# Kernel optimization log

Hardware: AMD Instinct MI355X
Metric: run time of the kernel (lower is better)

The kernel has to match this reference:

```python
import jax, jax.numpy as jnp
import numpy as np

B, S, HID = 2, 2048, 3584
NH, NKV, HD = 16, 8, 256
WINDOW = 1024
SOFTCAP = 50.0


def setup_inputs() -> dict:
    key = jax.random.key(0)
    ks = jax.random.split(key, 8)
    hidden_states = jax.random.normal(ks[0], (B, S, HID), dtype=jnp.float32)
    attention_mask = jnp.ones((B, S), dtype=bool)
    position_ids = jnp.tile(jnp.arange(S, dtype=jnp.int32), (B, 1))
    # rotary tables indexed by position, last dim = head_dim
    inv_freq = 1.0 / (10000.0 ** (jnp.arange(0, HD, 2, dtype=jnp.float32) / HD))
    t = jnp.arange(S, dtype=jnp.float32)
    freqs = jnp.outer(t, inv_freq)  # [S, HD/2]
    emb = jnp.concatenate([freqs, freqs], axis=-1)  # [S, HD]
    sin, cos = jnp.sin(emb), jnp.cos(emb)
    causal_mask = jnp.tril(jnp.ones((1, 1, S, S), dtype=bool))
    sc = 0.02
    Wq = jax.random.normal(ks[1], (HID, NH * HD), dtype=jnp.float32) * sc
    Wk = jax.random.normal(ks[2], (HID, NKV * HD), dtype=jnp.float32) * sc
    Wv = jax.random.normal(ks[3], (HID, NKV * HD), dtype=jnp.float32) * sc
    Wo = jax.random.normal(ks[4], (NH * HD, HID), dtype=jnp.float32) * sc
    return {"hidden_states": hidden_states, "attention_mask": attention_mask,
            "position_ids": position_ids, "sin": sin, "cos": cos,
            "causal_mask": causal_mask, "Wq": Wq, "Wk": Wk, "Wv": Wv, "Wo": Wo}


def _rotate_half(x):
    x1, x2 = x[..., : x.shape[-1] // 2], x[..., x.shape[-1] // 2 :]
    return jnp.concatenate((-x2, x1), axis=-1)


def reference(hidden_states, attention_mask, position_ids, sin, cos, causal_mask, Wq, Wk, Wv, Wo):
    b, s, _ = hidden_states.shape
    q = (hidden_states @ Wq).reshape(b, s, NH, HD)
    k = (hidden_states @ Wk).reshape(b, s, NKV, HD)
    v = (hidden_states @ Wv).reshape(b, s, NKV, HD)

    # RoPE, applied in [b, h, s, d] layout as in the original
    s_ = sin[position_ids][:, None, :, :]  # [b,1,s,d]
    c_ = cos[position_ids][:, None, :, :]
    qh = q.transpose(0, 2, 1, 3)
    kh = k.transpose(0, 2, 1, 3)
    qh = qh * c_ + _rotate_half(qh) * s_
    kh = kh * c_ + _rotate_half(kh) * s_
    q = qh.transpose(0, 2, 1, 3)  # [b,s,nh,d]
    k = kh.transpose(0, 2, 1, 3)  # [b,s,nkv,d]

    # GQA: repeat kv heads to match query heads
    groups = NH // NKV
    k = jnp.repeat(k, groups, axis=2)  # [b,s,nh,d]
    v = jnp.repeat(v, groups, axis=2)

    # combine causal + padding masks, then sliding-window (even layer)
    mask = causal_mask[:, :, :s, :s] & attention_mask[:, None, None, :]  # [b,1,s,s]
    mask = jnp.broadcast_to(mask, (b, 1, s, s))
    far_past = jnp.tril(jnp.ones((s, s), dtype=bool), k=-WINDOW)[None, None]
    mask = mask & ~far_past

    neg = jnp.finfo(jnp.float32).min
    bias = jnp.where(mask, 0.0, neg).astype(jnp.float32)

    scale = HD ** -0.5
    logits = jnp.einsum("bqhd,bkhd->bhqk", q, k) * scale
    # Gemma2 logit softcapping
    logits = SOFTCAP * jnp.tanh(logits / SOFTCAP)
    logits = logits + bias
    probs = jax.nn.softmax(logits, axis=-1)
    out = jnp.einsum("bhqk,bkhd->bqhd", probs, v)
    out = out.reshape(b, s, NH * HD)
    return out @ Wo
```

## Files before the change

kernel.cpp:

```cpp
#include <hip/hip_runtime.h>
#include <hip/hip_bf16.h>

typedef __bf16 bf16x8_t __attribute__((ext_vector_type(8)));
typedef __bf16 bf16x4_t __attribute__((ext_vector_type(4)));
typedef short s16x4_t  __attribute__((ext_vector_type(4)));
typedef float f32x4_t  __attribute__((ext_vector_type(4)));

#define NB 2
#define NS 2048
#define NHID 3584
#define NHEADS 16
#define NKVH 8
#define DH 256
#define WIN 1024

__device__ __forceinline__ float bf2f(ushort u) {
  union { unsigned v; float f; } x; x.v = ((unsigned)u) << 16; return x.f;
}
__device__ __forceinline__ ushort f2bf(float f) {
  unsigned x = __builtin_bit_cast(unsigned, f);
  unsigned r = (x + 0x7fffu + ((x >> 16) & 1u)) >> 16;
  return (ushort)r;
}

__device__ __forceinline__ void gload16(const void* g, void* l) {
  __builtin_amdgcn_global_load_lds((const __attribute__((address_space(1))) void*)g,
                                   (__attribute__((address_space(3))) void*)l, 16, 0, 0);
}

__device__ __forceinline__ f32x4_t mfma_pv(s16x4_t a, s16x4_t b, f32x4_t c) {
#if __has_builtin(__builtin_amdgcn_mfma_f32_16x16x16_bf16)
  return __builtin_amdgcn_mfma_f32_16x16x16_bf16(
      __builtin_bit_cast(bf16x4_t, a), __builtin_bit_cast(bf16x4_t, b), c, 0, 0, 0);
#else
  return __builtin_amdgcn_mfma_f32_16x16x16bf16_1k(a, b, c, 0, 0, 0);
#endif
}

__device__ __forceinline__ float pexp(float s) {
  float e = __expf(fminf(s * 0.0025f, 80.f));
  float th = __fdividef(e - 1.f, e + 1.f);
  return __expf(50.f * th);
}

__global__ __launch_bounds__(256) void f32_to_bf16_kernel(const float* __restrict__ in,
                                                          ushort* __restrict__ out, int n4) {
  int i = (int)blockIdx.x * 256 + (int)threadIdx.x;
  if (i < n4) {
    float4 v = ((const float4*)in)[i];
    ushort4 o;
    o.x = f2bf(v.x); o.y = f2bf(v.y); o.z = f2bf(v.z); o.w = f2bf(v.w);
    ((ushort4*)out)[i] = o;
  }
}

__global__ __launch_bounds__(256) void transpose_f32_bf16(const float* __restrict__ in,
                                                          ushort* __restrict__ out,
                                                          int R, int Cc) {
  __shared__ ushort tile[64][72];
  const int t = threadIdx.x;
  const int ct = Cc >> 6;
  const int by = blockIdx.x / ct;
  const int bx = blockIdx.x % ct;
  const int r0 = by << 6, c0 = bx << 6;
#pragma unroll
  for (int i = 0; i < 16; ++i) {
    int idx = i * 256 + t;
    int r = idx >> 6, c = idx & 63;
    tile[r][c] = f2bf(in[(size_t)(r0 + r) * Cc + c0 + c]);
  }
  __syncthreads();
#pragma unroll
  for (int i = 0; i < 16; ++i) {
    int idx = i * 256 + t;
    int rr = idx >> 6, cc = idx & 63;
    out[(size_t)(c0 + rr) * R + r0 + cc] = tile[cc][rr];
  }
}

#define GSYNC1 do { __builtin_amdgcn_s_barrier(); \
    asm volatile("s_waitcnt lgkmcnt(0)" ::: "memory"); \
    __builtin_amdgcn_sched_barrier(0); } while (0)
#define GSYNC2(st) do { \
    if (st) asm volatile("s_waitcnt vmcnt(2)" ::: "memory"); \
    else    asm volatile("s_waitcnt vmcnt(0)" ::: "memory"); \
    __builtin_amdgcn_sched_barrier(0); \
    __builtin_amdgcn_s_barrier(); } while (0)

template <int EPI>
__global__ __launch_bounds__(512, 2) void gemm256(const ushort* __restrict__ A,
                                                  const ushort* __restrict__ Bt,
                                                  void* __restrict__ Cout,
                                                  int M, int N, int K) {
  __shared__ alignas(16) char lds[131072];
  const int t = threadIdx.x;
  const int lane = t & 63;
  const int wid = t >> 6;
  const int wm = wid >> 2;
  const int wn = wid & 3;
  const int g = lane >> 4;
  const int lr = lane & 15;
  const int lrow8 = lane >> 3;
  const int lp = (lane & 7) ^ lrow8;

  const int nbn = N >> 8;
  const int nwg = (int)gridDim.x;
  const int bid = (int)blockIdx.x;
  const int swz = (bid & 7) * (nwg >> 3) + (bid >> 3);
  const int bm = swz / nbn, bn = swz % nbn;
  const int m0 = bm << 8, n0 = bn << 8;

  f32x4_t acc[8][4] = {};
  const int T = K >> 6;

  auto stageA = [&](int q, int koff, int bufn) {
    int row = (q << 6) + (wid << 3) + lrow8;
    gload16(A + (size_t)(m0 + row) * K + koff + (lp << 3),
            lds + bufn * 32768 + (q << 13) + (wid << 10));
  };
  auto stageB = [&](int q, int koff, int bufn) {
    int row = (q << 6) + (wid << 3) + lrow8;
    gload16(Bt + (size_t)(n0 + row) * K + koff + (lp << 3),
            lds + 65536 + bufn * 32768 + (q << 13) + (wid << 10));
  };

#pragma unroll
  for (int q = 0; q < 4; ++q) { stageA(q, 0, 0); stageB(q, 0, 0); }
  asm volatile("s_waitcnt vmcnt(0)" ::: "memory");
  __builtin_amdgcn_s_barrier();

  for (int tt = 0; tt < T; ++tt) {
    const int bc = tt & 1;
    const int bnx = bc ^ 1;
    const bool st = (tt + 1 < T);
    const int kn = (tt + 1) << 6;
    const char* cA = lds + bc * 32768;
    const char* cB = lds + 65536 + bc * 32768;
    bf16x8_t af[4], bfv[4];

    auto ldA = [&](int i, int mh, int ks) {
      int row = (wm << 7) + (mh << 6) + (i << 4) + lr;
      af[i] = *(const bf16x8_t*)(cA + (row << 7) + (((ks << 6) + (g << 4)) ^ ((row & 7) << 4)));
    };
    auto ldB = [&](int j, int ks) {
      int row = (wn << 6) + (j << 4) + lr;
      bfv[j] = *(const bf16x8_t*)(cB + (row << 7) + (((ks << 6) + (g << 4)) ^ ((row & 7) << 4)));
    };

#pragma unroll
    for (int i = 0; i < 4; ++i) ldA(i, 0, 0);
#pragma unroll
    for (int j = 0; j < 4; ++j) ldB(j, 0);
    if (st) { stageA(0, kn, bnx); stageA(2, kn, bnx); }
    GSYNC1;
    __builtin_amdgcn_s_setprio(1);
#pragma unroll
    for (int i = 0; i < 4; ++i)
#pragma unroll
      for (int j = 0; j < 4; ++j)
        acc[i][j] = __builtin_amdgcn_mfma_f32_16x16x32_bf16(af[i], bfv[j], acc[i][j], 0, 0, 0);
    __builtin_amdgcn_s_setprio(0);
    GSYNC2(st);

#pragma unroll
    for (int i = 0; i < 4; ++i) ldA(i, 1, 0);
    if (st) { stageB(0, kn, bnx); stageB(1, kn, bnx); }
    GSYNC1;
    __builtin_amdgcn_s_setprio(1);
#pragma unroll
    for (int i = 0; i < 4; ++i)
#pragma unroll
      for (int j = 0; j < 4; ++j)
        acc[4 + i][j] = __builtin_amdgcn_mfma_f32_16x16x32_bf16(af[i], bfv[j], acc[4 + i][j], 0, 0, 0);
    __builtin_amdgcn_s_setprio(0);
    GSYNC2(st);

#pragma unroll
    for (int i = 0; i < 4; ++i) ldA(i, 0, 1);
#pragma unroll
    for (int j = 0; j < 4; ++j) ldB(j, 1);
    if (st) { stageB(2, kn, bnx); stageB(3, kn, bnx); }
    GSYNC1;
    __builtin_amdgcn_s_setprio(1);
#pragma unroll
    for (int i = 0; i < 4; ++i)
#pragma unroll
      for (int j = 0; j < 4; ++j)
        acc[i][j] = __builtin_amdgcn_mfma_f32_16x16x32_bf16(af[i], bfv[j], acc[i][j], 0, 0, 0);
    __builtin_amdgcn_s_setprio(0);
    GSYNC2(st);

#pragma unroll
    for (int i = 0; i < 4; ++i) ldA(i, 1, 1);
    if (st) { stageA(1, kn, bnx); stageA(3, kn, bnx); }
    GSYNC1;
    __builtin_amdgcn_s_setprio(1);
#pragma unroll
    for (int i = 0; i < 4; ++i)
#pragma unroll
      for (int j = 0; j < 4; ++j)
        acc[4 + i][j] = __builtin_amdgcn_mfma_f32_16x16x32_bf16(af[i], bfv[j], acc[4 + i][j], 0, 0, 0);
    __builtin_amdgcn_s_setprio(0);
    GSYNC2(st);
  }

  __syncthreads();
  const bool trstage = (EPI == 4) && (n0 >= 2048);
  if (trstage) {
#pragma unroll
    for (int i = 0; i < 8; ++i)
#pragma unroll
      for (int j = 0; j < 4; ++j) {
        int col = (wn << 6) + (j << 4) + lr;
#pragma unroll
        for (int r = 0; r < 4; ++r) {
          int row = (wm << 7) + (i << 4) + (g << 2) + r;
          *(ushort*)(lds + (col << 9) + ((row << 1) ^ ((col & 7) << 4))) = f2bf(acc[i][j][r]);
        }
      }
  } else {
#pragma unroll
    for (int i = 0; i < 8; ++i)
#pragma unroll
      for (int j = 0; j < 4; ++j) {
        int col = (wn << 6) + (j << 4) + lr;
#pragma unroll
        for (int r = 0; r < 4; ++r) {
          int row = (wm << 7) + (i << 4) + (g << 2) + r;
          *(ushort*)(lds + (row << 9) + ((col << 1) ^ ((row & 7) << 4))) = f2bf(acc[i][j][r]);
        }
      }
  }
  __syncthreads();

  if (EPI == 0) {
    ushort* C = (ushort*)Cout;
#pragma unroll
    for (int it = 0; it < 16; ++it) {
      int idx = it * 512 + t;
      int row = idx >> 5, ch = idx & 31;
      uint4 v = *(const uint4*)(lds + (row << 9) + ((ch << 4) ^ ((row & 7) << 4)));
      *(uint4*)(C + (size_t)(m0 + row) * N + n0 + (ch << 3)) = v;
    }
  } else if (EPI == 4) {
    ushort* C = (ushort*)Cout;
    if (n0 < 2048) {
#pragma unroll
      for (int it = 0; it < 16; ++it) {
        int idx = it * 512 + t;
        int row = idx >> 5, ch = idx & 31;
        uint4 v = *(const uint4*)(lds + (row << 9) + ((ch << 4) ^ ((row & 7) << 4)));
        *(uint4*)(C + (size_t)(m0 + row) * 2048 + n0 + (ch << 3)) = v;
      }
    } else {
      ushort* vC = C + (size_t)4096 * 2048;
      const int plane = (m0 >> 11) * NKVH + ((n0 - 2048) >> 8);
      ushort* dst = vC + (size_t)plane * ((size_t)NS * DH) + (size_t)((m0 & (NS - 1)) >> 5) * 8192;
#pragma unroll
      for (int it = 0; it < 16; ++it) {
        int s = it * 512 + t;
        int lr2 = s & 7, kq = (s >> 3) & 7, dt_l = (s >> 6) & 15, sb_l = s >> 10;
        int d0 = (dt_l << 4) + (lr2 << 1);
        int r0 = (sb_l << 5) + (kq << 2);
        uint2 a = *(const uint2*)(lds + (d0 << 9) + ((r0 << 1) ^ ((d0 & 7) << 4)));
        uint2 b2 = *(const uint2*)(lds + ((d0 + 1) << 9) + ((r0 << 1) ^ (((d0 + 1) & 7) << 4)));
        uint4 v; v.x = a.x; v.y = a.y; v.z = b2.x; v.w = b2.y;
        *(uint4*)(dst + (size_t)s * 8) = v;
      }
    }
  } else {
    float* Cf = (float*)Cout;
#pragma unroll
    for (int it = 0; it < 32; ++it) {
      int idx = it * 512 + t;
      int row = idx >> 6, qd = idx & 63;
      ushort4 hv = *(const ushort4*)(lds + (row << 9) + ((qd << 3) ^ ((row & 7) << 4)));
      float4 fv;
      fv.x = bf2f(hv.x); fv.y = bf2f(hv.y); fv.z = bf2f(hv.z); fv.w = bf2f(hv.w);
      *(float4*)(Cf + (size_t)(m0 + row) * N + n0 + (qd << 2)) = fv;
    }
  }
}

__global__ __launch_bounds__(256) void rope_kernel(ushort* __restrict__ buf,
                                                   const float* __restrict__ sint,
                                                   const float* __restrict__ cost,
                                                   int nheads) {
  int idx = (int)blockIdx.x * 256 + (int)threadIdx.x;
  int d = idx & 127;
  int h = (idx >> 7) % nheads;
  int tok = idx / (nheads << 7);
  int pos = tok & (NS - 1);
  float c = cost[pos * DH + d];
  float s = sint[pos * DH + d];
  size_t base = (size_t)tok * ((size_t)nheads * DH) + h * DH + d;
  float x1 = bf2f(buf[base]);
  float x2 = bf2f(buf[base + 128]);
  buf[base] = f2bf(x1 * c - x2 * s);
  buf[base + 128] = f2bf(x2 * c + x1 * s);
}

__global__ __launch_bounds__(512) void attn_kernel(const ushort* __restrict__ q,
                                                   const ushort* __restrict__ k,
                                                   const ushort* __restrict__ vt,
                                                   ushort* __restrict__ ao) {
  __shared__ alignas(16) char lK[2][16384];
  __shared__ alignas(16) char lV[2][16384];
  const int bid = (int)blockIdx.x;
  const int qb = bid & 15;
  const int h = (bid >> 4) & 15;
  const int b = bid >> 8;
  const int kvh = h >> 1;
  const int qb0 = qb << 7;
  const int t = threadIdx.x;
  const int lane = t & 63;
  const int w = t >> 6;
  const int g = lane >> 4;
  const int lr = lane & 15;

  const int qrow = qb0 + (w << 4) + lr;
  bf16x8_t qf[8];
  const ushort* qbase = q + (size_t)(b * NS + qrow) * (NHEADS * DH) + h * DH;
#pragma unroll
  for (int ks = 0; ks < 8; ++ks)
    qf[ks] = *(const bf16x8_t*)(qbase + (ks << 5) + (g << 3));

  float l_r = 0.f;
  f32x4_t oacc[16] = {};

  const int qminw = qb0 + (w << 4);
  const int qmaxw = qminw + 15;
  int t_lo = qb0 - (WIN - 1);
  if (t_lo < 0) t_lo = 0;
  t_lo &= ~31;
  const int t_hi = qb0 + 127;
  const int nt = ((t_hi - t_lo) >> 5) + 1;

  const ushort* kgb = k + (size_t)(b * NS) * (NKVH * DH) + kvh * DH;
  const ushort* vgb = vt + (size_t)(b * NKVH + kvh) * ((size_t)NS * DH);

  auto stage = [&](int kt, int bi) {
    char* dk = lK[bi];
    char* dv = lV[bi];
    const int sb = kt >> 5;
#pragma unroll
    for (int j = 0; j < 2; ++j) {
      int i = (w << 1) + j;
      int row = (i << 1) + (lane >> 5);
      int ck = (lane & 31) ^ (row & 7);
      gload16(kgb + (size_t)(kt + row) * (NKVH * DH) + (ck << 3), dk + (i << 10));
      gload16(vgb + (size_t)sb * 8192 + (((i << 6) + lane) << 3), dv + (i << 10));
    }
  };

  int cur = 0;
  stage(t_lo, 0);
  __syncthreads();

  for (int i = 0; i < nt; ++i) {
    const int kt = t_lo + (i << 5);
    if (i + 1 < nt) stage(kt + 32, cur ^ 1);
    const char* lk = lK[cur];
    const char* lv = lV[cur];
#pragma unroll
    for (int sub = 0; sub < 2; ++sub) {
      const int key0 = kt + (sub << 4);
      if (key0 > qmaxw) continue;
      if (key0 + 15 < qminw - (WIN - 1)) continue;

      f32x4_t sacc = {};
      __builtin_amdgcn_s_setprio(1);
#pragma unroll
      for (int ks = 0; ks < 8; ++ks) {
        int row = (sub << 4) + lr;
        bf16x8_t kf = *(const bf16x8_t*)(lk + (((row << 9) + (ks << 6) + (g << 4)) ^ ((row & 7) << 4)));
        sacc = __builtin_amdgcn_mfma_f32_16x16x32_bf16(kf, qf[ks], sacc, 0, 0, 0);
      }
      __builtin_amdgcn_s_setprio(0);

      float pvv[4];
      const bool full = (key0 + 15 <= qminw) && (key0 >= qmaxw - (WIN - 1));
      if (full) {
#pragma unroll
        for (int r = 0; r < 4; ++r) { pvv[r] = pexp(sacc[r]); l_r += pvv[r]; }
      } else {
#pragma unroll
        for (int r = 0; r < 4; ++r) {
          int key = key0 + (g << 2) + r;
          bool ok = (key <= qrow) && (qrow - key < WIN);
          pvv[r] = ok ? pexp(sacc[r]) : 0.f;
          l_r += pvv[r];
        }
      }

      s16x4_t pa;
      pa[0] = (short)f2bf(pvv[0]);
      pa[1] = (short)f2bf(pvv[1]);
      pa[2] = (short)f2bf(pvv[2]);
      pa[3] = (short)f2bf(pvv[3]);

      const int kqoff = ((sub << 2) + g) << 7;
      __builtin_amdgcn_s_setprio(1);
#pragma unroll
      for (int dt = 0; dt < 16; ++dt) {
        s16x4_t vf = *(const s16x4_t*)(lv + (dt << 10) + kqoff + (lr << 3));
        oacc[dt] = mfma_pv(pa, vf, oacc[dt]);
      }
      __builtin_amdgcn_s_setprio(0);
    }
    __syncthreads();
    cur ^= 1;
  }

  l_r += __shfl_xor(l_r, 16);
  l_r += __shfl_xor(l_r, 32);
  float dn[4];
#pragma unroll
  for (int r = 0; r < 4; ++r)
    dn[r] = 1.0f / __shfl(l_r, (g << 2) + r);

  const int orow0 = b * NS + qb0 + (w << 4) + (g << 2);
#pragma unroll
  for (int dt = 0; dt < 16; ++dt) {
    int col = h * DH + (dt << 4) + lr;
#pragma unroll
    for (int r = 0; r < 4; ++r) {
      ao[(size_t)(orow0 + r) * (NHEADS * DH) + col] = f2bf(oacc[dt][r] * dn[r]);
    }
  }
}

extern "C" void kernel_launch(void* const* d_in, const int* in_sizes, int n_in,
                              void* d_out, int out_size, void* d_ws, size_t ws_size,
                              hipStream_t stream) {
  const float* hs   = (const float*)d_in[0];
  const float* sint = (const float*)d_in[3];
  const float* cost = (const float*)d_in[4];
  const float* Wq = (const float*)d_in[6];
  const float* Wk = (const float*)d_in[7];
  const float* Wv = (const float*)d_in[8];
  const float* Wo = (const float*)d_in[9];

  char* ws = (char*)d_ws;
  size_t off = 0;
  auto alloc = [&](size_t bytes) {
    char* p = ws + off;
    off += (bytes + 255) & ~(size_t)255;
    return p;
  };
  ushort* hsb   = (ushort*)alloc((size_t)4096 * 3584 * 2);
  ushort* wT    = (ushort*)alloc((size_t)4096 * 3584 * 2);
  ushort* qbuf  = (ushort*)alloc((size_t)4096 * 4096 * 2);
  ushort* kbuf  = (ushort*)alloc((size_t)4096 * 2048 * 2);
  ushort* vtbuf = (ushort*)alloc((size_t)4096 * 2048 * 2);
  ushort* aobuf = qbuf;
  if (off > ws_size) return;

  f32_to_bf16_kernel<<<(4096 * 3584 / 4) / 256, 256, 0, stream>>>(hs, hsb, 4096 * 3584 / 4);

  transpose_f32_bf16<<<(3584 / 64) * (2048 / 64), 256, 0, stream>>>(Wk, wT, 3584, 2048);
  transpose_f32_bf16<<<(3584 / 64) * (2048 / 64), 256, 0, stream>>>(Wv, wT + (size_t)2048 * 3584, 3584, 2048);
  gemm256<4><<<16 * 16, 512, 0, stream>>>(hsb, wT, kbuf, 4096, 4096, 3584);

  transpose_f32_bf16<<<(3584 / 64) * (4096 / 64), 256, 0, stream>>>(Wq, wT, 3584, 4096);
  gemm256<0><<<16 * 16, 512, 0, stream>>>(hsb, wT, qbuf, 4096, 4096, 3584);

  rope_kernel<<<(4096 * 16 * 128) / 256, 256, 0, stream>>>(qbuf, sint, cost, 16);
  rope_kernel<<<(4096 * 8 * 128) / 256, 256, 0, stream>>>(kbuf, sint, cost, 8);

  attn_kernel<<<NB * NHEADS * (NS / 128), 512, 0, stream>>>(qbuf, kbuf, vtbuf, aobuf);

  transpose_f32_bf16<<<(4096 / 64) * (3584 / 64), 256, 0, stream>>>(Wo, wT, 4096, 3584);
  gemm256<2><<<16 * 14, 512, 0, stream>>>(aobuf, wT, d_out, 4096, 3584, 4096);
}
```

Before: 603.1 us.

## Shrink attention tiles, read V directly from global, remap blocks for XCD locality

The attention kernel now processes 64 query rows per block with 256 threads instead of 128 rows with 512, and doubles the grid. It stops staging V tiles in LDS and loads pre-transposed V fragments straight from global memory inside the PV MFMA loop, keeping only K double-buffered in shared memory. Block indices are remapped so blocks sharing a KV head land on the same XCD, and query-block order is flipped to balance causal work. The aim is more occupancy and better L2 reuse, traded against global-load latency on the PV path and less intra-block K reuse.

```diff
diff --git a/kernel.cpp b/kernel.cpp
--- a/kernel.cpp
+++ b/kernel.cpp
@@ -300,18 +300,24 @@
   buf[base + 128] = f2bf(x2 * c + x1 * s);
 }
 
-__global__ __launch_bounds__(512) void attn_kernel(const ushort* __restrict__ q,
-                                                   const ushort* __restrict__ k,
-                                                   const ushort* __restrict__ vt,
-                                                   ushort* __restrict__ ao) {
+__global__ __launch_bounds__(256, 4) void attn_kernel(const ushort* __restrict__ q,
+                                                      const ushort* __restrict__ k,
+                                                      const ushort* __restrict__ vt,
+                                                      ushort* __restrict__ ao) {
   __shared__ alignas(16) char lK[2][16384];
-  __shared__ alignas(16) char lV[2][16384];
   const int bid = (int)blockIdx.x;
-  const int qb = bid & 15;
-  const int h = (bid >> 4) & 15;
-  const int b = bid >> 8;
-  const int kvh = h >> 1;
-  const int qb0 = qb << 7;
+  const int xcd = bid & 7;
+  const int idx = bid >> 3;
+  const int flip = idx & 1;
+  const int h_lsb = (idx >> 1) & 1;
+  const int plane_hi = (idx >> 2) & 1;
+  const int qb_base = idx >> 3;
+  const int qb = flip ? 31 - qb_base : qb_base;
+  const int plane = xcd + (plane_hi << 3);
+  const int b = plane >> 3;
+  const int kvh = plane & 7;
+  const int h = (kvh << 1) | h_lsb;
+  const int qb0 = qb << 6;
   const int t = threadIdx.x;
   const int lane = t & 63;
   const int w = t >> 6;
@@ -333,35 +339,32 @@
   int t_lo = qb0 - (WIN - 1);
   if (t_lo < 0) t_lo = 0;
   t_lo &= ~31;
-  const int t_hi = qb0 + 127;
+  const int t_hi = qb0 + 63;
   const int nt = ((t_hi - t_lo) >> 5) + 1;
 
   const ushort* kgb = k + (size_t)(b * NS) * (NKVH * DH) + kvh * DH;
   const ushort* vgb = vt + (size_t)(b * NKVH + kvh) * ((size_t)NS * DH);
 
-  auto stage = [&](int kt, int bi) {
+  auto stageK = [&](int kt, int bi) {
     char* dk = lK[bi];
-    char* dv = lV[bi];
-    const int sb = kt >> 5;
-#pragma unroll
-    for (int j = 0; j < 2; ++j) {
-      int i = (w << 1) + j;
-      int row = (i << 1) + (lane >> 5);
+#pragma unroll
+    for (int j = 0; j < 4; ++j) {
+      int row = (w << 3) + (j << 1) + (lane >> 5);
       int ck = (lane & 31) ^ (row & 7);
-      gload16(kgb + (size_t)(kt + row) * (NKVH * DH) + (ck << 3), dk + (i << 10));
-      gload16(vgb + (size_t)sb * 8192 + (((i << 6) + lane) << 3), dv + (i << 10));
+      gload16(kgb + (size_t)(kt + row) * (NKVH * DH) + (ck << 3),
+              dk + (((w << 3) + (j << 1)) << 9));
     }
   };
 
   int cur = 0;
-  stage(t_lo, 0);
+  stageK(t_lo, 0);
   __syncthreads();
 
   for (int i = 0; i < nt; ++i) {
     const int kt = t_lo + (i << 5);
-    if (i + 1 < nt) stage(kt + 32, cur ^ 1);
+    if (i + 1 < nt) stageK(kt + 32, cur ^ 1);
     const char* lk = lK[cur];
-    const char* lv = lV[cur];
+    const ushort* vtile = vgb + (size_t)(kt >> 5) * 8192;
 #pragma unroll
     for (int sub = 0; sub < 2; ++sub) {
       const int key0 = kt + (sub << 4);
@@ -399,11 +402,11 @@
       pa[2] = (short)f2bf(pvv[2]);
       pa[3] = (short)f2bf(pvv[3]);
 
-      const int kqoff = ((sub << 2) + g) << 7;
+      const int voff = (((sub << 2) + g) << 6) + (lr << 2);
       __builtin_amdgcn_s_setprio(1);
 #pragma unroll
       for (int dt = 0; dt < 16; ++dt) {
-        s16x4_t vf = *(const s16x4_t*)(lv + (dt << 10) + kqoff + (lr << 3));
+        s16x4_t vf = *(const s16x4_t*)(vtile + (dt << 9) + voff);
         oacc[dt] = mfma_pv(pa, vf, oacc[dt]);
       }
       __builtin_amdgcn_s_setprio(0);
@@ -468,7 +471,7 @@
   rope_kernel<<<(4096 * 16 * 128) / 256, 256, 0, stream>>>(qbuf, sint, cost, 16);
   rope_kernel<<<(4096 * 8 * 128) / 256, 256, 0, stream>>>(kbuf, sint, cost, 8);
 
-  attn_kernel<<<NB * NHEADS * (NS / 128), 512, 0, stream>>>(qbuf, kbuf, vtbuf, aobuf);
+  attn_kernel<<<NB * NHEADS * (NS / 64), 256, 0, stream>>>(qbuf, kbuf, vtbuf, aobuf);
 
   transpose_f32_bf16<<<(4096 / 64) * (3584 / 64), 256, 0, stream>>>(Wo, wT, 4096, 3584);
   gemm256<2><<<16 * 14, 512, 0, stream>>>(aobuf, wT, d_out, 4096, 3584, 4096);
```

Result: slower. 815.4 us (+35.2%).
